# Performance work log

Hardware: AMD Instinct MI355X
Metric: run time of the kernel (lower is better)

The kernel has to match this reference:

```python
import jax, jax.numpy as jnp
import numpy as np

DIM_OUT = 64


def setup_inputs() -> dict:
    key = jax.random.key(0)
    k1, k2, k3, k4 = jax.random.split(key, 4)
    B, N, D_in, D_out = 4, 4096, 512, DIM_OUT
    x = jax.random.normal(k1, (B, N, D_in), dtype=jnp.float32)
    s = 1.0 / np.sqrt(D_in)
    Wk = jax.random.normal(k2, (D_out, D_in), dtype=jnp.float32) * s
    Wq = jax.random.normal(k3, (D_out, D_in), dtype=jnp.float32) * s
    Wv = jax.random.normal(k4, (D_out, D_in), dtype=jnp.float32) * s
    return {"x": x, "Wk": Wk, "Wq": Wq, "Wv": Wv}


def reference(x, Wk, Wq, Wv):
    # x: [B, N, D_in]; W*: [D_out, D_in] (torch Linear, no bias -> x @ W.T)
    keys = jnp.einsum('bnd,od->bno', x, Wk)
    queries = jnp.einsum('bnd,od->bno', x, Wq)
    values = jnp.einsum('bnd,od->bno', x, Wv)
    d_out = Wk.shape[0]
    # causal attention scores: [B, N, N]
    scores = jnp.einsum('bio,bjo->bij', queries, keys) / jnp.sqrt(jnp.float32(d_out))
    N = x.shape[1]
    causal = jnp.tril(jnp.ones((N, N), dtype=bool))  # [N, N]
    scores = jnp.where(causal[None, :, :], scores, -jnp.inf)
    att = jax.nn.softmax(scores, axis=-1)
    return jnp.einsum('bjo,bij->bio', values, att)
```

## Files before the change

### kernel.cpp

```cpp
#include <hip/hip_runtime.h>
#include <hip/hip_bf16.h>
#include <math.h>

#define N_   4096
#define DIN  512
#define D_   64

typedef __attribute__((ext_vector_type(8))) short  bf16x8;
typedef __attribute__((ext_vector_type(4))) float  f32x4;

#define ZERO4 ((f32x4){0.f, 0.f, 0.f, 0.f})

__device__ __forceinline__ unsigned short bf16rne(float x) {
    unsigned u = __float_as_uint(x);
    return (unsigned short)((u + 0x7FFFu + ((u >> 16) & 1u)) >> 16);
}
__device__ __forceinline__ unsigned cvt2(float a, float b) {
    __hip_bfloat162 h = __float22bfloat162_rn(make_float2(a, b));
    unsigned u; __builtin_memcpy(&u, &h, 4);
    return u;
}
__device__ __forceinline__ uint2 cvt4(float4 v) {
    return make_uint2(cvt2(v.x, v.y), cvt2(v.z, v.w));
}
__device__ __forceinline__ void pl32swap(unsigned &a, unsigned &b) {
    asm volatile("v_permlane32_swap_b32 %0, %1" : "+v"(a), "+v"(b));
}
__device__ __forceinline__ void pl16swap(unsigned &a, unsigned &b) {
    asm volatile("v_permlane16_swap_b32 %0, %1" : "+v"(a), "+v"(b));
}
__device__ __forceinline__ int swz(int row, int byte_in_row) {
    return (row * 128 + (byte_in_row ^ ((row & 7) << 4))) >> 1;
}

#define GLD16(gp, lp)                                                          \
    __builtin_amdgcn_global_load_lds(                                          \
        (const __attribute__((address_space(1))) unsigned int*)(gp),           \
        (__attribute__((address_space(3))) unsigned int*)(lp), 16, 0, 0)

__device__ __forceinline__ int pb64(int qi) {
    const int k = qi >> 4;
    return qi + 16 * (k * (k - 1) / 2) + (qi & 15) * k;
}
#define PART64_F 4160

__global__ __launch_bounds__(512) void proj_kernel(
    const float* __restrict__ X, const float* __restrict__ Wk,
    const float* __restrict__ Wq, const float* __restrict__ Wv,
    unsigned short* __restrict__ Kb, unsigned short* __restrict__ Qb,
    unsigned short* __restrict__ Vt)
{
    __shared__ unsigned short Xs[2][64 * 64];
    __shared__ unsigned short Ws[2][192 * 64];

    const int tid  = threadIdx.x;
    const int lane = tid & 63;
    const int w    = tid >> 6;
    const int q15  = lane & 15;
    const int hi   = lane >> 4;
    const int rt   = w >> 1;
    const int oh   = w & 1;
    const int rbase = blockIdx.x * 64;

    float4 xr[2], wr[6];

    auto loadT = [&](int kc) {
        #pragma unroll
        for (int i = 0; i < 2; ++i) {
            const int idx = tid + i * 512;
            xr[i] = *(const float4*)(X + (size_t)(rbase + (idx >> 4)) * DIN + kc + (idx & 15) * 4);
        }
        #pragma unroll
        for (int i = 0; i < 6; ++i) {
            const int idx  = tid + i * 512;
            const int wrow = idx >> 4;
            const float* Wp = (wrow < 64)  ? Wk + (size_t)wrow * DIN
                            : (wrow < 128) ? Wq + (size_t)(wrow - 64) * DIN
                                           : Wv + (size_t)(wrow - 128) * DIN;
            wr[i] = *(const float4*)(Wp + kc + (idx & 15) * 4);
        }
    };
    auto storeT = [&](int p) {
        #pragma unroll
        for (int i = 0; i < 2; ++i) {
            const int idx = tid + i * 512;
            *(uint2*)&Xs[p][swz(idx >> 4, (idx & 15) * 8)] = cvt4(xr[i]);
        }
        #pragma unroll
        for (int i = 0; i < 6; ++i) {
            const int idx = tid + i * 512;
            *(uint2*)&Ws[p][swz(idx >> 4, (idx & 15) * 8)] = cvt4(wr[i]);
        }
    };

    f32x4 acc[6];
    #pragma unroll
    for (int i = 0; i < 6; ++i) acc[i] = ZERO4;

    loadT(0);
    int p = 0;
    for (int it = 0; it < 8; ++it) {
        storeT(p);
        __syncthreads();
        if (it < 7) loadT((it + 1) * 64);
        #pragma unroll
        for (int ks = 0; ks < 2; ++ks) {
            bf16x8 af = *(const bf16x8*)&Xs[p][swz(rt * 16 + q15, ks * 64 + hi * 16)];
            #pragma unroll
            for (int j = 0; j < 6; ++j) {
                bf16x8 bfr = *(const bf16x8*)&Ws[p][swz((oh * 6 + j) * 16 + q15, ks * 64 + hi * 16)];
                acc[j] = __builtin_amdgcn_mfma_f32_16x16x32_bf16(af, bfr, acc[j], 0, 0, 0);
            }
        }
        p ^= 1;
    }

    unsigned short* Os = &Ws[0][0];
    #pragma unroll
    for (int j = 0; j < 6; ++j) {
        const int og = oh * 6 + j;
        #pragma unroll
        for (int r = 0; r < 4; ++r) {
            const int n = rt * 16 + hi * 4 + r;
            const int o = og * 16 + q15;
            unsigned short v = bf16rne(acc[j][r]);
            if (og < 4)      Kb[(size_t)(rbase + n) * D_ + o]        = v;
            else if (og < 8) Qb[(size_t)(rbase + n) * D_ + (o - 64)] = v;
            else             Os[n * 66 + (o - 128)]                  = v;
        }
    }
    __syncthreads();
    {
        const int o  = tid >> 3;
        const int ng = (tid & 7) * 8;
        unsigned short tmp[8];
        #pragma unroll
        for (int i = 0; i < 8; ++i) tmp[i] = Os[(ng + i) * 66 + o];
        const int b  = rbase >> 12;
        const int nb = rbase & (N_ - 1);
        *(uint4*)(Vt + ((size_t)b * D_ + o) * N_ + nb + ng) = *(uint4*)&tmp[0];
    }
}

__global__ __launch_bounds__(256) void attn_part_kernel(
    const unsigned short* __restrict__ Qb, const unsigned short* __restrict__ Kb,
    const unsigned short* __restrict__ Vt, float* __restrict__ Pws)
{
    __shared__ unsigned short Ks[2][64 * 64];
    __shared__ unsigned short Vs[2][64 * 64];

    const int tid  = threadIdx.x;
    const int lane = tid & 63;
    const int w    = tid >> 6;
    const int q15  = lane & 15;
    const int hi   = lane >> 4;

    const int b = blockIdx.x & 3;
    const int u = blockIdx.x >> 2;
    int sl, qi;
    if      (u < 64)  { sl = 0; qi = 63 - u; }
    else if (u < 112) { sl = 1; qi = 63 - (u - 64); }
    else if (u < 144) { sl = 2; qi = 63 - (u - 112); }
    else              { sl = 3; qi = 63 - (u - 144); }
    const int nch  = qi + 1;
    const int cbeg = sl * 16;
    const int cend = min(nch, cbeg + 16);
    const int qb   = qi * 64;

    const unsigned short* Qp = Qb + (size_t)b * N_ * D_;
    const unsigned short* Kp = Kb + (size_t)b * N_ * D_;
    const unsigned short* Vp = Vt + (size_t)b * D_ * N_;

    const int qg = qb + w * 16 + q15;
    bf16x8 qf[2];
    #pragma unroll
    for (int ks = 0; ks < 2; ++ks)
        qf[ks] = *(const bf16x8*)(Qp + (size_t)qg * D_ + ks * 32 + hi * 8);

    f32x4 accO[4];
    #pragma unroll
    for (int dt = 0; dt < 4; ++dt) accO[dt] = ZERO4;
    float lsum = 0.f;

    const int lsw = 8 * ((lane & 7) ^ (lane >> 3));

    auto issueChunk = [&](int p, int c) {
        const int kb2 = c * 64;
        #pragma unroll
        for (int i = 0; i < 2; ++i) {
            const int r8  = w * 2 + i;
            const int row = r8 * 8 + (lane >> 3);
            GLD16(Kp + (size_t)(kb2 + row) * D_ + lsw, &Ks[p][r8 * 512]);
            GLD16(Vp + (size_t)row * N_ + kb2 + lsw,   &Vs[p][r8 * 512]);
        }
    };

    issueChunk(0, cbeg);
    __syncthreads();

    const float SC = 0.125f * 1.44269504f;
    int p = 0;

    for (int c = cbeg; c < cend; ++c) {
        if (c + 1 < cend) issueChunk(p ^ 1, c + 1);
        const int kbase = c * 64;
        const bool edge = (c == nch - 1);

        f32x4 sv[4];
        #pragma unroll
        for (int kt = 0; kt < 4; ++kt) {
            bf16x8 k0 = *(const bf16x8*)&Ks[p][swz(kt * 16 + q15, hi * 16)];
            bf16x8 k1 = *(const bf16x8*)&Ks[p][swz(kt * 16 + q15, 64 + hi * 16)];
            sv[kt] = __builtin_amdgcn_mfma_f32_16x16x32_bf16(k0, qf[0], ZERO4, 0, 0, 0);
            sv[kt] = __builtin_amdgcn_mfma_f32_16x16x32_bf16(k1, qf[1], sv[kt], 0, 0, 0);
        }

        unsigned pk[4][2];
        #pragma unroll
        for (int kt = 0; kt < 4; ++kt) {
            float pv[4];
            #pragma unroll
            for (int r = 0; r < 4; ++r) {
                float vv = sv[kt][r] * SC;
                const int kg = kbase + kt * 16 + hi * 4 + r;
                if (edge) vv = (kg <= qg) ? vv : -INFINITY;
                pv[r] = __builtin_amdgcn_exp2f(vv);
                lsum += pv[r];
            }
            pk[kt][0] = cvt2(pv[0], pv[1]);
            pk[kt][1] = cvt2(pv[2], pv[3]);
        }

        #pragma unroll
        for (int ks2 = 0; ks2 < 2; ++ks2) {
            unsigned a0 = pk[2 * ks2][0],     a1 = pk[2 * ks2][1];
            unsigned b0 = pk[2 * ks2 + 1][0], b1 = pk[2 * ks2 + 1][1];
            pl32swap(a0, b0);
            pl32swap(a1, b1);
            pl16swap(a0, b0);
            pl16swap(a1, b1);
            unsigned pw[4] = {a0, a1, b0, b1};
            bf16x8 pa;
            __builtin_memcpy(&pa, pw, 16);
            #pragma unroll
            for (int dt = 0; dt < 4; ++dt) {
                bf16x8 vf = *(const bf16x8*)&Vs[p][swz(dt * 16 + q15, ks2 * 64 + hi * 16)];
                accO[dt] = __builtin_amdgcn_mfma_f32_16x16x32_bf16(pa, vf, accO[dt], 0, 0, 0);
            }
        }

        __syncthreads();
        p ^= 1;
    }

    lsum += __shfl_xor(lsum, 16);
    lsum += __shfl_xor(lsum, 32);

    float* partO = Pws + ((size_t)b * 160 + pb64(qi) + sl) * PART64_F;
    #pragma unroll
    for (int dt = 0; dt < 4; ++dt)
        #pragma unroll
        for (int r = 0; r < 4; ++r)
            partO[(w * 16 + hi * 4 + r) * 64 + dt * 16 + q15] = accO[dt][r];
    if (hi == 0) partO[4096 + w * 16 + q15] = lsum;
}

__global__ __launch_bounds__(256) void attn_merge_kernel(
    const float* __restrict__ Pws, float* __restrict__ O)
{
    const int tid = threadIdx.x;
    const int b   = blockIdx.x & 3;
    const int qi  = blockIdx.x >> 2;
    const int np  = (qi + 16) >> 4;
    const float* base = Pws + ((size_t)b * 160 + pb64(qi)) * PART64_F;

    const int q  = tid >> 2;
    const int dg = (tid & 3) * 16;

    float s[16];
    #pragma unroll
    for (int i = 0; i < 16; ++i) s[i] = 0.f;
    float L = 0.f;
    for (int pp = 0; pp < np; ++pp) {
        const float* sp = base + (size_t)pp * PART64_F + q * 64 + dg;
        #pragma unroll
        for (int i = 0; i < 4; ++i) {
            float4 v = *(const float4*)(sp + i * 4);
            s[4*i]   += v.x; s[4*i+1] += v.y;
            s[4*i+2] += v.z; s[4*i+3] += v.w;
        }
        L += base[(size_t)pp * PART64_F + 4096 + q];
    }
    const float rL = 1.0f / L;
    float* dst = O + ((size_t)b * N_ + qi * 64 + q) * D_ + dg;
    #pragma unroll
    for (int i = 0; i < 4; ++i)
        *(float4*)(dst + i * 4) = make_float4(s[4*i] * rL, s[4*i+1] * rL,
                                              s[4*i+2] * rL, s[4*i+3] * rL);
}

extern "C" void kernel_launch(void* const* d_in, const int* in_sizes, int n_in,
                              void* d_out, int out_size, void* d_ws, size_t ws_size,
                              hipStream_t stream)
{
    const float* x  = (const float*)d_in[0];
    const float* Wk = (const float*)d_in[1];
    const float* Wq = (const float*)d_in[2];
    const float* Wv = (const float*)d_in[3];
    float* O = (float*)d_out;

    const size_t per = (size_t)4 * N_ * D_;
    unsigned short* Kb = (unsigned short*)d_ws;
    unsigned short* Qb = Kb + per;
    unsigned short* Vt = Qb + per;
    float* Pws = (float*)((char*)d_ws + 3 * per * sizeof(unsigned short));

    proj_kernel<<<dim3(4 * N_ / 64), 512, 0, stream>>>(x, Wk, Wq, Wv, Kb, Qb, Vt);
    attn_part_kernel<<<dim3(640), 256, 0, stream>>>(Qb, Kb, Vt, Pws);
    attn_merge_kernel<<<dim3(256), 256, 0, stream>>>(Pws, O);
}
```

Measured before the change: 50.49 us.

## Pre-convert weights to bf16 and stream them to LDS via direct global loads

```diff
diff --git a/kernel.cpp b/kernel.cpp
--- a/kernel.cpp
+++ b/kernel.cpp
@@ -44,14 +44,27 @@
 }
 #define PART64_F 4160
 
-__global__ __launch_bounds__(512) void proj_kernel(
-    const float* __restrict__ X, const float* __restrict__ Wk,
-    const float* __restrict__ Wq, const float* __restrict__ Wv,
+__global__ __launch_bounds__(256) void wcvt_kernel(
+    const float* __restrict__ Wk, const float* __restrict__ Wq,
+    const float* __restrict__ Wv, unsigned short* __restrict__ Wb)
+{
+    const int idx = (blockIdx.x * 256 + threadIdx.x) * 4;
+    const int row = idx >> 9;
+    const int col = idx & 511;
+    const float* src = (row < 64)  ? Wk + (size_t)row * 512 + col
+                     : (row < 128) ? Wq + (size_t)(row - 64) * 512 + col
+                                   : Wv + (size_t)(row - 128) * 512 + col;
+    float4 v = *(const float4*)src;
+    *(uint2*)&Wb[idx] = cvt4(v);
+}
+
+__global__ __launch_bounds__(256) void proj_kernel(
+    const float* __restrict__ X, const unsigned short* __restrict__ Wb,
     unsigned short* __restrict__ Kb, unsigned short* __restrict__ Qb,
     unsigned short* __restrict__ Vt)
 {
-    __shared__ unsigned short Xs[2][64 * 64];
-    __shared__ unsigned short Ws[2][192 * 64];
+    __shared__ unsigned short Wl[2][192 * 64];
+    __shared__ unsigned short Xs[2][32 * 64];
 
     const int tid  = threadIdx.x;
     const int lane = tid & 63;
@@ -60,62 +73,62 @@
     const int hi   = lane >> 4;
     const int rt   = w >> 1;
     const int oh   = w & 1;
-    const int rbase = blockIdx.x * 64;
-
-    float4 xr[2], wr[6];
-
-    auto loadT = [&](int kc) {
+    const int rbase = blockIdx.x * 32;
+
+    const int lsw = 8 * ((lane & 7) ^ (lane >> 3));
+
+    auto issueW = [&](int p, int kc) {
+        #pragma unroll
+        for (int i = 0; i < 6; ++i) {
+            const int r8  = w * 6 + i;
+            const int row = r8 * 8 + (lane >> 3);
+            GLD16(Wb + (size_t)row * DIN + kc + lsw, &Wl[p][r8 * 512]);
+        }
+    };
+
+    float4 xr[2];
+    auto loadX = [&](int kc) {
         #pragma unroll
         for (int i = 0; i < 2; ++i) {
-            const int idx = tid + i * 512;
+            const int idx = tid + i * 256;
             xr[i] = *(const float4*)(X + (size_t)(rbase + (idx >> 4)) * DIN + kc + (idx & 15) * 4);
         }
-        #pragma unroll
-        for (int i = 0; i < 6; ++i) {
-            const int idx  = tid + i * 512;
-            const int wrow = idx >> 4;
-            const float* Wp = (wrow < 64)  ? Wk + (size_t)wrow * DIN
-                            : (wrow < 128) ? Wq + (size_t)(wrow - 64) * DIN
-                                           : Wv + (size_t)(wrow - 128) * DIN;
-            wr[i] = *(const float4*)(Wp + kc + (idx & 15) * 4);
-        }
     };
-    auto storeT = [&](int p) {
+    auto storeX = [&](int p) {
         #pragma unroll
         for (int i = 0; i < 2; ++i) {
-            const int idx = tid + i * 512;
+            const int idx = tid + i * 256;
             *(uint2*)&Xs[p][swz(idx >> 4, (idx & 15) * 8)] = cvt4(xr[i]);
         }
-        #pragma unroll
-        for (int i = 0; i < 6; ++i) {
-            const int idx = tid + i * 512;
-            *(uint2*)&Ws[p][swz(idx >> 4, (idx & 15) * 8)] = cvt4(wr[i]);
-        }
     };
 
     f32x4 acc[6];
     #pragma unroll
     for (int i = 0; i < 6; ++i) acc[i] = ZERO4;
 
-    loadT(0);
+    loadX(0);
+    issueW(0, 0);
+    storeX(0);
+    __syncthreads();
     int p = 0;
     for (int it = 0; it < 8; ++it) {
-        storeT(p);
-        __syncthreads();
-        if (it < 7) loadT((it + 1) * 64);
+        if (it < 7) { loadX((it + 1) * 64); issueW(p ^ 1, (it + 1) * 64); }
         #pragma unroll
         for (int ks = 0; ks < 2; ++ks) {
             bf16x8 af = *(const bf16x8*)&Xs[p][swz(rt * 16 + q15, ks * 64 + hi * 16)];
             #pragma unroll
             for (int j = 0; j < 6; ++j) {
-                bf16x8 bfr = *(const bf16x8*)&Ws[p][swz((oh * 6 + j) * 16 + q15, ks * 64 + hi * 16)];
+                bf16x8 bfr = *(const bf16x8*)&Wl[p][swz((oh * 6 + j) * 16 + q15, ks * 64 + hi * 16)];
                 acc[j] = __builtin_amdgcn_mfma_f32_16x16x32_bf16(af, bfr, acc[j], 0, 0, 0);
             }
         }
+        __syncthreads();
+        if (it < 7) storeX(p ^ 1);
+        __syncthreads();
         p ^= 1;
     }
 
-    unsigned short* Os = &Ws[0][0];
+    unsigned short* Os = &Xs[0][0];
     #pragma unroll
     for (int j = 0; j < 6; ++j) {
         const int og = oh * 6 + j;
@@ -131,8 +144,8 @@
     }
     __syncthreads();
     {
-        const int o  = tid >> 3;
-        const int ng = (tid & 7) * 8;
+        const int o  = tid >> 2;
+        const int ng = (tid & 3) * 8;
         unsigned short tmp[8];
         #pragma unroll
         for (int i = 0; i < 8; ++i) tmp[i] = Os[(ng + i) * 66 + o];
@@ -313,9 +326,11 @@
     unsigned short* Kb = (unsigned short*)d_ws;
     unsigned short* Qb = Kb + per;
     unsigned short* Vt = Qb + per;
-    float* Pws = (float*)((char*)d_ws + 3 * per * sizeof(unsigned short));
-
-    proj_kernel<<<dim3(4 * N_ / 64), 512, 0, stream>>>(x, Wk, Wq, Wv, Kb, Qb, Vt);
+    unsigned short* Wb = Vt + per;
+    float* Pws = (float*)((char*)d_ws + (3 * per + 192 * 512) * sizeof(unsigned short));
+
+    wcvt_kernel<<<dim3(96), 256, 0, stream>>>(Wk, Wq, Wv, Wb);
+    proj_kernel<<<dim3(4 * N_ / 32), 256, 0, stream>>>(x, Wb, Kb, Qb, Vt);
     attn_part_kernel<<<dim3(640), 256, 0, stream>>>(Qb, Kb, Vt, Pws);
     attn_merge_kernel<<<dim3(256), 256, 0, stream>>>(Pws, O);
 }
```

Result: slower. 55.36 us (+9.7%).

## Use single-wave attention blocks covering all 64 queries and prescale Q in projection

Applied to the files above, without the earlier changes.

```diff
diff --git a/kernel.cpp b/kernel.cpp
--- a/kernel.cpp
+++ b/kernel.cpp
@@ -43,6 +43,8 @@
     return qi + 16 * (k * (k - 1) / 2) + (qi & 15) * k;
 }
 #define PART64_F 4160
+
+#define SCQ 0.18033688f
 
 __global__ __launch_bounds__(512) void proj_kernel(
     const float* __restrict__ X, const float* __restrict__ Wk,
@@ -123,10 +125,9 @@
         for (int r = 0; r < 4; ++r) {
             const int n = rt * 16 + hi * 4 + r;
             const int o = og * 16 + q15;
-            unsigned short v = bf16rne(acc[j][r]);
-            if (og < 4)      Kb[(size_t)(rbase + n) * D_ + o]        = v;
-            else if (og < 8) Qb[(size_t)(rbase + n) * D_ + (o - 64)] = v;
-            else             Os[n * 66 + (o - 128)]                  = v;
+            if (og < 4)      Kb[(size_t)(rbase + n) * D_ + o]        = bf16rne(acc[j][r]);
+            else if (og < 8) Qb[(size_t)(rbase + n) * D_ + (o - 64)] = bf16rne(acc[j][r] * SCQ);
+            else             Os[n * 66 + (o - 128)]                  = bf16rne(acc[j][r]);
         }
     }
     __syncthreads();
@@ -142,16 +143,14 @@
     }
 }
 
-__global__ __launch_bounds__(256) void attn_part_kernel(
+__global__ __launch_bounds__(64) void attn_part_kernel(
     const unsigned short* __restrict__ Qb, const unsigned short* __restrict__ Kb,
     const unsigned short* __restrict__ Vt, float* __restrict__ Pws)
 {
     __shared__ unsigned short Ks[2][64 * 64];
     __shared__ unsigned short Vs[2][64 * 64];
 
-    const int tid  = threadIdx.x;
-    const int lane = tid & 63;
-    const int w    = tid >> 6;
+    const int lane = threadIdx.x & 63;
     const int q15  = lane & 15;
     const int hi   = lane >> 4;
 
@@ -171,81 +170,94 @@
     const unsigned short* Kp = Kb + (size_t)b * N_ * D_;
     const unsigned short* Vp = Vt + (size_t)b * D_ * N_;
 
-    const int qg = qb + w * 16 + q15;
-    bf16x8 qf[2];
-    #pragma unroll
-    for (int ks = 0; ks < 2; ++ks)
-        qf[ks] = *(const bf16x8*)(Qp + (size_t)qg * D_ + ks * 32 + hi * 8);
-
-    f32x4 accO[4];
-    #pragma unroll
-    for (int dt = 0; dt < 4; ++dt) accO[dt] = ZERO4;
-    float lsum = 0.f;
+    bf16x8 qf[4][2];
+    #pragma unroll
+    for (int s = 0; s < 4; ++s)
+        #pragma unroll
+        for (int ks = 0; ks < 2; ++ks)
+            qf[s][ks] = *(const bf16x8*)(Qp + (size_t)(qb + s * 16 + q15) * D_ + ks * 32 + hi * 8);
+
+    f32x4 accO[4][4];
+    #pragma unroll
+    for (int s = 0; s < 4; ++s)
+        #pragma unroll
+        for (int dt = 0; dt < 4; ++dt) accO[s][dt] = ZERO4;
+    float lsum[4] = {0.f, 0.f, 0.f, 0.f};
 
     const int lsw = 8 * ((lane & 7) ^ (lane >> 3));
 
     auto issueChunk = [&](int p, int c) {
         const int kb2 = c * 64;
         #pragma unroll
-        for (int i = 0; i < 2; ++i) {
-            const int r8  = w * 2 + i;
-            const int row = r8 * 8 + (lane >> 3);
-            GLD16(Kp + (size_t)(kb2 + row) * D_ + lsw, &Ks[p][r8 * 512]);
-            GLD16(Vp + (size_t)row * N_ + kb2 + lsw,   &Vs[p][r8 * 512]);
+        for (int i = 0; i < 8; ++i) {
+            const int row = i * 8 + (lane >> 3);
+            GLD16(Kp + (size_t)(kb2 + row) * D_ + lsw, &Ks[p][i * 512]);
+            GLD16(Vp + (size_t)row * N_ + kb2 + lsw,   &Vs[p][i * 512]);
         }
     };
 
     issueChunk(0, cbeg);
     __syncthreads();
 
-    const float SC = 0.125f * 1.44269504f;
     int p = 0;
-
     for (int c = cbeg; c < cend; ++c) {
-        if (c + 1 < cend) issueChunk(p ^ 1, c + 1);
         const int kbase = c * 64;
         const bool edge = (c == nch - 1);
 
-        f32x4 sv[4];
+        f32x4 sv[4][4];
         #pragma unroll
         for (int kt = 0; kt < 4; ++kt) {
             bf16x8 k0 = *(const bf16x8*)&Ks[p][swz(kt * 16 + q15, hi * 16)];
             bf16x8 k1 = *(const bf16x8*)&Ks[p][swz(kt * 16 + q15, 64 + hi * 16)];
-            sv[kt] = __builtin_amdgcn_mfma_f32_16x16x32_bf16(k0, qf[0], ZERO4, 0, 0, 0);
-            sv[kt] = __builtin_amdgcn_mfma_f32_16x16x32_bf16(k1, qf[1], sv[kt], 0, 0, 0);
-        }
-
-        unsigned pk[4][2];
-        #pragma unroll
-        for (int kt = 0; kt < 4; ++kt) {
-            float pv[4];
-            #pragma unroll
-            for (int r = 0; r < 4; ++r) {
-                float vv = sv[kt][r] * SC;
-                const int kg = kbase + kt * 16 + hi * 4 + r;
-                if (edge) vv = (kg <= qg) ? vv : -INFINITY;
-                pv[r] = __builtin_amdgcn_exp2f(vv);
-                lsum += pv[r];
-            }
-            pk[kt][0] = cvt2(pv[0], pv[1]);
-            pk[kt][1] = cvt2(pv[2], pv[3]);
+            #pragma unroll
+            for (int s = 0; s < 4; ++s) {
+                sv[s][kt] = __builtin_amdgcn_mfma_f32_16x16x32_bf16(k0, qf[s][0], ZERO4, 0, 0, 0);
+                sv[s][kt] = __builtin_amdgcn_mfma_f32_16x16x32_bf16(k1, qf[s][1], sv[s][kt], 0, 0, 0);
+            }
+        }
+
+        if (c + 1 < cend) issueChunk(p ^ 1, c + 1);
+
+        unsigned pk[4][4][2];
+        #pragma unroll
+        for (int s = 0; s < 4; ++s) {
+            const int qg = qb + s * 16 + q15;
+            #pragma unroll
+            for (int kt = 0; kt < 4; ++kt) {
+                float pv[4];
+                #pragma unroll
+                for (int r = 0; r < 4; ++r) {
+                    float vv = sv[s][kt][r];
+                    const int kg = kbase + kt * 16 + hi * 4 + r;
+                    if (edge) vv = (kg <= qg) ? vv : -INFINITY;
+                    pv[r] = __builtin_amdgcn_exp2f(vv);
+                    lsum[s] += pv[r];
+                }
+                pk[s][kt][0] = cvt2(pv[0], pv[1]);
+                pk[s][kt][1] = cvt2(pv[2], pv[3]);
+            }
         }
 
         #pragma unroll
         for (int ks2 = 0; ks2 < 2; ++ks2) {
-            unsigned a0 = pk[2 * ks2][0],     a1 = pk[2 * ks2][1];
-            unsigned b0 = pk[2 * ks2 + 1][0], b1 = pk[2 * ks2 + 1][1];
-            pl32swap(a0, b0);
-            pl32swap(a1, b1);
-            pl16swap(a0, b0);
-            pl16swap(a1, b1);
-            unsigned pw[4] = {a0, a1, b0, b1};
-            bf16x8 pa;
-            __builtin_memcpy(&pa, pw, 16);
+            bf16x8 pa[4];
+            #pragma unroll
+            for (int s = 0; s < 4; ++s) {
+                unsigned a0 = pk[s][2 * ks2][0],     a1 = pk[s][2 * ks2][1];
+                unsigned b0 = pk[s][2 * ks2 + 1][0], b1 = pk[s][2 * ks2 + 1][1];
+                pl32swap(a0, b0);
+                pl32swap(a1, b1);
+                pl16swap(a0, b0);
+                pl16swap(a1, b1);
+                unsigned pw[4] = {a0, a1, b0, b1};
+                __builtin_memcpy(&pa[s], pw, 16);
+            }
             #pragma unroll
             for (int dt = 0; dt < 4; ++dt) {
                 bf16x8 vf = *(const bf16x8*)&Vs[p][swz(dt * 16 + q15, ks2 * 64 + hi * 16)];
-                accO[dt] = __builtin_amdgcn_mfma_f32_16x16x32_bf16(pa, vf, accO[dt], 0, 0, 0);
+                #pragma unroll
+                for (int s = 0; s < 4; ++s)
+                    accO[s][dt] = __builtin_amdgcn_mfma_f32_16x16x32_bf16(pa[s], vf, accO[s][dt], 0, 0, 0);
             }
         }
 
@@ -253,16 +265,22 @@
         p ^= 1;
     }
 
-    lsum += __shfl_xor(lsum, 16);
-    lsum += __shfl_xor(lsum, 32);
+    #pragma unroll
+    for (int s = 0; s < 4; ++s) {
+        lsum[s] += __shfl_xor(lsum[s], 16);
+        lsum[s] += __shfl_xor(lsum[s], 32);
+    }
 
     float* partO = Pws + ((size_t)b * 160 + pb64(qi) + sl) * PART64_F;
     #pragma unroll
-    for (int dt = 0; dt < 4; ++dt)
-        #pragma unroll
-        for (int r = 0; r < 4; ++r)
-            partO[(w * 16 + hi * 4 + r) * 64 + dt * 16 + q15] = accO[dt][r];
-    if (hi == 0) partO[4096 + w * 16 + q15] = lsum;
+    for (int s = 0; s < 4; ++s) {
+        #pragma unroll
+        for (int dt = 0; dt < 4; ++dt)
+            #pragma unroll
+            for (int r = 0; r < 4; ++r)
+                partO[(s * 16 + hi * 4 + r) * 64 + dt * 16 + q15] = accO[s][dt][r];
+        if (hi == 0) partO[4096 + s * 16 + q15] = lsum[s];
+    }
 }
 
 __global__ __launch_bounds__(256) void attn_merge_kernel(
@@ -316,6 +334,6 @@
     float* Pws = (float*)((char*)d_ws + 3 * per * sizeof(unsigned short));
 
     proj_kernel<<<dim3(4 * N_ / 64), 512, 0, stream>>>(x, Wk, Wq, Wv, Kb, Qb, Vt);
-    attn_part_kernel<<<dim3(640), 256, 0, stream>>>(Qb, Kb, Vt, Pws);
+    attn_part_kernel<<<dim3(640), 64, 0, stream>>>(Qb, Kb, Vt, Pws);
     attn_merge_kernel<<<dim3(256), 256, 0, stream>>>(Pws, O);
 }
```

Result: slower. 61.89 us (+22.6%).

## Split causal KV range into 8-chunk slices and prefold softmax scale into Q

Applied to the files above, without the earlier changes.

```diff
diff --git a/kernel.cpp b/kernel.cpp
--- a/kernel.cpp
+++ b/kernel.cpp
@@ -38,11 +38,13 @@
         (const __attribute__((address_space(1))) unsigned int*)(gp),           \
         (__attribute__((address_space(3))) unsigned int*)(lp), 16, 0, 0)
 
-__device__ __forceinline__ int pb64(int qi) {
-    const int k = qi >> 4;
-    return qi + 16 * (k * (k - 1) / 2) + (qi & 15) * k;
+__device__ __forceinline__ int pb8(int qi) {
+    const int g = qi >> 3, r = qi & 7;
+    return 4 * g * (g + 1) + r * (g + 1);
 }
 #define PART64_F 4160
+
+#define SCQ 0.18033688f
 
 __global__ __launch_bounds__(512) void proj_kernel(
     const float* __restrict__ X, const float* __restrict__ Wk,
@@ -123,10 +125,9 @@
         for (int r = 0; r < 4; ++r) {
             const int n = rt * 16 + hi * 4 + r;
             const int o = og * 16 + q15;
-            unsigned short v = bf16rne(acc[j][r]);
-            if (og < 4)      Kb[(size_t)(rbase + n) * D_ + o]        = v;
-            else if (og < 8) Qb[(size_t)(rbase + n) * D_ + (o - 64)] = v;
-            else             Os[n * 66 + (o - 128)]                  = v;
+            if (og < 4)      Kb[(size_t)(rbase + n) * D_ + o]        = bf16rne(acc[j][r]);
+            else if (og < 8) Qb[(size_t)(rbase + n) * D_ + (o - 64)] = bf16rne(acc[j][r] * SCQ);
+            else             Os[n * 66 + (o - 128)]                  = bf16rne(acc[j][r]);
         }
     }
     __syncthreads();
@@ -157,14 +158,19 @@
 
     const int b = blockIdx.x & 3;
     const int u = blockIdx.x >> 2;
-    int sl, qi;
-    if      (u < 64)  { sl = 0; qi = 63 - u; }
-    else if (u < 112) { sl = 1; qi = 63 - (u - 64); }
-    else if (u < 144) { sl = 2; qi = 63 - (u - 112); }
-    else              { sl = 3; qi = 63 - (u - 144); }
+    const int v = 287 - u;
+    int g = 0;
+    #pragma unroll
+    for (int t = 1; t < 8; ++t)
+        if (4 * t * (t + 1) <= v) g = t;
+    const int idx = v - 4 * g * (g + 1);
+    const int qs  = idx / (g + 1);
+    const int qi  = 8 * g + qs;
+    const int sl  = idx - qs * (g + 1);
+
     const int nch  = qi + 1;
-    const int cbeg = sl * 16;
-    const int cend = min(nch, cbeg + 16);
+    const int cbeg = sl * 8;
+    const int cend = min(nch, cbeg + 8);
     const int qb   = qi * 64;
 
     const unsigned short* Qp = Qb + (size_t)b * N_ * D_;
@@ -198,9 +204,7 @@
     issueChunk(0, cbeg);
     __syncthreads();
 
-    const float SC = 0.125f * 1.44269504f;
     int p = 0;
-
     for (int c = cbeg; c < cend; ++c) {
         if (c + 1 < cend) issueChunk(p ^ 1, c + 1);
         const int kbase = c * 64;
@@ -221,7 +225,7 @@
             float pv[4];
             #pragma unroll
             for (int r = 0; r < 4; ++r) {
-                float vv = sv[kt][r] * SC;
+                float vv = sv[kt][r];
                 const int kg = kbase + kt * 16 + hi * 4 + r;
                 if (edge) vv = (kg <= qg) ? vv : -INFINITY;
                 pv[r] = __builtin_amdgcn_exp2f(vv);
@@ -256,7 +260,7 @@
     lsum += __shfl_xor(lsum, 16);
     lsum += __shfl_xor(lsum, 32);
 
-    float* partO = Pws + ((size_t)b * 160 + pb64(qi) + sl) * PART64_F;
+    float* partO = Pws + ((size_t)b * 288 + pb8(qi) + sl) * PART64_F;
     #pragma unroll
     for (int dt = 0; dt < 4; ++dt)
         #pragma unroll
@@ -271,8 +275,8 @@
     const int tid = threadIdx.x;
     const int b   = blockIdx.x & 3;
     const int qi  = blockIdx.x >> 2;
-    const int np  = (qi + 16) >> 4;
-    const float* base = Pws + ((size_t)b * 160 + pb64(qi)) * PART64_F;
+    const int np  = (qi + 8) >> 3;
+    const float* base = Pws + ((size_t)b * 288 + pb8(qi)) * PART64_F;
 
     const int q  = tid >> 2;
     const int dg = (tid & 3) * 16;
@@ -316,6 +320,6 @@
     float* Pws = (float*)((char*)d_ws + 3 * per * sizeof(unsigned short));
 
     proj_kernel<<<dim3(4 * N_ / 64), 512, 0, stream>>>(x, Wk, Wq, Wv, Kb, Qb, Vt);
-    attn_part_kernel<<<dim3(640), 256, 0, stream>>>(Qb, Kb, Vt, Pws);
+    attn_part_kernel<<<dim3(1152), 256, 0, stream>>>(Qb, Kb, Vt, Pws);
     attn_merge_kernel<<<dim3(256), 256, 0, stream>>>(Pws, O);
 }
```

Result: no change. 50.07 us (-0.8%).
